# Kernel tuning notes

Measured on AMD Instinct MI355X. Metric: run time of the kernel, lower is better.

## Reference

```python
import jax, jax.numpy as jnp
import numpy as np

# 3x3 laplacian stencil, OIHW
LAP = jnp.array([-1, -1, -1, -1, 8, -1, -1, -1, -1], dtype=jnp.float32).reshape(1, 1, 3, 3)
THR = 0.1
SMOOTH = 1.0


def _lap_conv(x, stride):
    # x: [B,1,H,W]
    return jax.lax.conv_general_dilated(
        x, LAP, window_strides=(stride, stride), padding=((1, 1), (1, 1)),
        dimension_numbers=('NCHW', 'OIHW', 'NCHW'))


def _nearest_up(x, H, W):
    # PyTorch 'nearest': src_idx = floor(dst_idx * in/out)
    h, w = x.shape[2], x.shape[3]
    ri = (jnp.arange(H) * h) // H
    ci = (jnp.arange(W) * w) // W
    return x[:, :, ri][:, :, :, ci]


def _thresh(x):
    return jnp.where(x > THR, 1.0, 0.0).astype(x.dtype)


def setup_inputs() -> dict:
    key = jax.random.key(0)
    k1, k2 = jax.random.split(key)
    B, H, W = 16, 1024, 1024
    boundary_logits = jax.random.normal(k1, (B, 1, H, W), dtype=jnp.float32)
    gtmasks = (jax.random.uniform(k2, (B, H, W)) > 0.5).astype(jnp.float32)
    fuse_kernel = jnp.array([0.6, 0.3, 0.1], dtype=jnp.float32).reshape(1, 3, 1, 1)
    return {"boundary_logits": boundary_logits, "gtmasks": gtmasks, "fuse_kernel": fuse_kernel}


def reference(boundary_logits, gtmasks, fuse_kernel):
    g = gtmasks[:, None, :, :].astype(jnp.float32)  # [B,1,H,W]
    bt = _thresh(jnp.maximum(_lap_conv(g, 1), 0.0))  # full res
    H, W = bt.shape[2], bt.shape[3]
    bt2 = _thresh(_nearest_up(jnp.maximum(_lap_conv(g, 2), 0.0), H, W))
    bt4 = _thresh(_nearest_up(jnp.maximum(_lap_conv(g, 4), 0.0), H, W))
    # (x8 branch in original is computed but unused in the output)
    pyr = jnp.concatenate([bt, bt2, bt4], axis=1)  # [B,3,H,W]
    fused = jnp.einsum('bchw,c->bhw', pyr, fuse_kernel.reshape(3))[:, None]  # 1x1 fuse conv
    target = _thresh(fused)  # [B,1,H,W]

    x = boundary_logits
    # stable BCE with logits, mean reduction
    bce_loss = jnp.mean(jnp.maximum(x, 0.0) - x * target + jnp.log1p(jnp.exp(-jnp.abs(x))))

    p = jax.nn.sigmoid(x)
    n = p.shape[0]
    pf = p.reshape(n, -1)
    tf = target.reshape(n, -1)
    inter = jnp.sum(pf * tf, axis=1)
    dice_loss = jnp.mean(1.0 - (2.0 * inter + SMOOTH) / (jnp.sum(pf, 1) + jnp.sum(tf, 1) + SMOOTH))
    return bce_loss, dice_loss
```

## Files before the change

### kernel.cpp

```cpp
#include <hip/hip_runtime.h>

#define IMG_H 1024
#define IMG_W 1024
#define NIMG  16
#define NPIX  16777216.0f
#define NBLK  2048
#define LOG2E 1.44269504088896340736f
#define LN2   0.69314718055994530942f

#ifndef __has_builtin
#define __has_builtin(x) 0
#endif

__device__ __forceinline__ void stage16(const float* src, float* dstLds, int lane) {
#if __has_builtin(__builtin_amdgcn_global_load_lds)
    __builtin_amdgcn_global_load_lds(
        (const __attribute__((address_space(1))) void*)src,
        (__attribute__((address_space(3))) void*)dstLds,
        16, 0, 0);
#else
    *reinterpret_cast<float4*>(dstLds + (lane << 2)) =
        *reinterpret_cast<const float4*>(src);
#endif
}


__global__ __launch_bounds__(256, 4) void dal_main(
    const float* __restrict__ xlogits,
    const float* __restrict__ gmask,
    const float* __restrict__ fuse,
    float4* __restrict__ ws4)
{
    __shared__ float lds[10 * 1024];

    const int b    = blockIdx.x;
    const int img  = b >> 7;
    const int r0   = (b & 127) << 3;
    const int tid  = (int)threadIdx.x;
    const int wid  = tid >> 6;
    const int lane = tid & 63;
    const int j0   = tid * 4;

    const float w0 = fuse[0], w1 = fuse[1], w2 = fuse[2];

    const size_t ibase = (size_t)img * (IMG_H * IMG_W);
    const float* gi = gmask + ibase;
    const float* xi = xlogits + ibase;

    #pragma unroll
    for (int t = 0; t < 10; ++t) {
        int r  = r0 - 1 + t;
        int rc = r < 0 ? 0 : (r > IMG_H - 1 ? IMG_H - 1 : r);
        stage16(gi + (size_t)rc * IMG_W + j0, &lds[t * 1024 + (wid << 8)], lane);
    }

    float4 xv[8];
    const float* xr = xi + (size_t)r0 * IMG_W + j0;
    #pragma unroll
    for (int r = 0; r < 8; ++r)
        xv[r] = *reinterpret_cast<const float4*>(xr + (size_t)r * IMG_W);

    __syncthreads();

    const bool hasL = (j0 > 0);
    const bool hasR = (j0 + 4 < IMG_W);
    const int  jl   = hasL ? j0 - 1 : 0;
    const int  jr   = hasR ? j0 + 4 : IMG_W - 1;

    auto fold = [&](int t, float* rm, float* cvo) {
        const float* Lr = &lds[t * 1024];
        float4 v   = *reinterpret_cast<const float4*>(Lr + j0);
        float  lf0 = Lr[jl];
        float  rg0 = Lr[jr];
        float  lf  = hasL ? lf0 : 0.f;
        float  rg  = hasR ? rg0 : 0.f;
        rm[0] = fminf(lf,  fminf(v.x, v.y));
        rm[1] = fminf(v.x, fminf(v.y, v.z));
        rm[2] = fminf(v.y, fminf(v.z, v.w));
        rm[3] = fminf(v.z, fminf(v.w, rg));
        cvo[0] = v.x; cvo[1] = v.y; cvo[2] = v.z; cvo[3] = v.w;
    };

    float l2[2]  = {0.f, 0.f}, xt[2] = {0.f, 0.f};
    float itr[2] = {0.f, 0.f}, sp[2] = {0.f, 0.f};
    int st = 0;

    auto px = [&](float x, float btv, float b2v, int a) {
        float f = fmaf(w0, btv, b2v);
        bool  c = f > 0.1f;
        st += (int)__popcll(__ballot(c));
        float u   = __builtin_amdgcn_exp2f(x * LOG2E);
        float opu = 1.f + u;
        float p   = u * __builtin_amdgcn_rcpf(opu);
        l2[a]  += __builtin_amdgcn_logf(opu);
        sp[a]  += p;
        xt[a]  += c ? x : 0.f;
        itr[a] += c ? p : 0.f;
    };

    float rm0[4], rm1[4], rm2[4], rm3[4], cvA[4], cvB[4], cvC[4], tmp[4];
    fold(0, rm0, tmp);
    if (r0 == 0) { rm0[0] = rm0[1] = rm0[2] = rm0[3] = 0.f; }
    fold(1, rm1, cvA);
    float wb4A = 0.f, wb4B = 0.f;

    #pragma unroll
    for (int rp = 0; rp < 4; ++rp) {
        fold(2 * rp + 2, rm2, cvB);
        fold(2 * rp + 3, rm3, cvC);
        if (rp == 3 && r0 == IMG_H - 8) {
            rm3[0] = rm3[1] = rm3[2] = rm3[3] = 0.f;
        }

        float bta[4], btb[4];
        #pragma unroll
        for (int k = 0; k < 4; ++k) {
            float cma = fminf(rm0[k], fminf(rm1[k], rm2[k]));
            float cmb = fminf(rm1[k], fminf(rm2[k], rm3[k]));
            bta[k] = (cvA[k] > 0.5f && cma < 0.5f) ? 1.f : 0.f;
            btb[k] = (cvB[k] > 0.5f && cmb < 0.5f) ? 1.f : 0.f;
        }
        if (rp == 0) wb4A = w2 * bta[0];
        if (rp == 2) wb4B = w2 * bta[0];
        const float wb  = (rp < 2) ? wb4A : wb4B;
        const float b20 = fmaf(w1, bta[0], wb);
        const float b21 = fmaf(w1, bta[2], wb);

        px(xv[2 * rp].x,     bta[0], b20, 0);
        px(xv[2 * rp].y,     bta[1], b20, 0);
        px(xv[2 * rp].z,     bta[2], b21, 0);
        px(xv[2 * rp].w,     bta[3], b21, 0);
        px(xv[2 * rp + 1].x, btb[0], b20, 1);
        px(xv[2 * rp + 1].y, btb[1], b20, 1);
        px(xv[2 * rp + 1].z, btb[2], b21, 1);
        px(xv[2 * rp + 1].w, btb[3], b21, 1);

        #pragma unroll
        for (int k = 0; k < 4; ++k) {
            rm0[k] = rm2[k]; rm1[k] = rm3[k]; cvA[k] = cvC[k];
        }
    }

    float bce   = fmaf(LN2, l2[0] + l2[1], -(xt[0] + xt[1]));
    float inter = itr[0] + itr[1];
    float sump  = sp[0] + sp[1];

    #pragma unroll
    for (int off = 32; off > 0; off >>= 1) {
        bce   += __shfl_down(bce, off);
        inter += __shfl_down(inter, off);
        sump  += __shfl_down(sump, off);
    }
    __syncthreads();
    if (lane == 0) {
        lds[wid]      = bce;
        lds[4 + wid]  = inter;
        lds[8 + wid]  = sump;
        lds[12 + wid] = (float)st;
    }
    __syncthreads();
    if (tid == 0) {
        float4 o;
        o.x = (lds[0]  + lds[1])  + (lds[2]  + lds[3]);
        o.y = (lds[4]  + lds[5])  + (lds[6]  + lds[7]);
        o.z = (lds[8]  + lds[9])  + (lds[10] + lds[11]);
        o.w = (lds[12] + lds[13]) + (lds[14] + lds[15]);
        ws4[b] = o;
    }
}

__global__ __launch_bounds__(1024) void dal_finalize(
    const float4* __restrict__ ws4, float* __restrict__ out)
{
    const int t    = (int)threadIdx.x;
    const int wv   = t >> 6;
    const int lane = t & 63;

    float4 a = ws4[2 * t];
    float4 bq = ws4[2 * t + 1];
    float bce   = a.x + bq.x;
    float inter = a.y + bq.y;
    float sump  = a.z + bq.z;
    float sumt  = a.w + bq.w;

    #pragma unroll
    for (int off = 32; off > 0; off >>= 1) {
        bce   += __shfl_down(bce, off);
        inter += __shfl_down(inter, off);
        sump  += __shfl_down(sump, off);
        sumt  += __shfl_down(sumt, off);
    }

    __shared__ float sb[16], sd[16];
    if (lane == 0) {
        sb[wv] = bce;
        sd[wv] = 1.f - (2.f * inter + 1.f) / (sump + sumt + 1.f);
    }
    __syncthreads();
    if (t == 0) {
        float tb = 0.f, td = 0.f;
        #pragma unroll
        for (int i = 0; i < NIMG; ++i) { tb += sb[i]; td += sd[i]; }
        out[0] = tb / NPIX;
        out[1] = td / (float)NIMG;
    }
}

extern "C" void kernel_launch(void* const* d_in, const int* in_sizes, int n_in,
                              void* d_out, int out_size, void* d_ws, size_t ws_size,
                              hipStream_t stream)
{
    const float* x    = (const float*)d_in[0];
    const float* g    = (const float*)d_in[1];
    const float* fuse = (const float*)d_in[2];
    float* out = (float*)d_out;
    float4* ws4 = (float4*)d_ws;

    dal_main<<<NBLK, 256, 0, stream>>>(x, g, fuse, ws4);
    dal_finalize<<<1, 1024, 0, stream>>>(ws4, out);
}
```

Baseline: 32.09 us.

## Halve rows per block, swizzle blocks across XCDs, raise occupancy

```diff
diff --git a/kernel.cpp b/kernel.cpp
--- a/kernel.cpp
+++ b/kernel.cpp
@@ -4,7 +4,7 @@
 #define IMG_W 1024
 #define NIMG  16
 #define NPIX  16777216.0f
-#define NBLK  2048
+#define NBLK  4096
 #define LOG2E 1.44269504088896340736f
 #define LN2   0.69314718055994530942f
 
@@ -25,17 +25,19 @@
 }
 
 
-__global__ __launch_bounds__(256, 4) void dal_main(
+__global__ __launch_bounds__(256, 6) void dal_main(
     const float* __restrict__ xlogits,
     const float* __restrict__ gmask,
     const float* __restrict__ fuse,
     float4* __restrict__ ws4)
 {
-    __shared__ float lds[10 * 1024];
-
-    const int b    = blockIdx.x;
-    const int img  = b >> 7;
-    const int r0   = (b & 127) << 3;
+    __shared__ float lds[6 * 1024];
+
+    const int bid = blockIdx.x;
+    const int b   = (bid & 7) * (NBLK / 8) + (bid >> 3);
+
+    const int img  = b >> 8;
+    const int r0   = (b & 255) << 2;
     const int tid  = (int)threadIdx.x;
     const int wid  = tid >> 6;
     const int lane = tid & 63;
@@ -48,16 +50,16 @@
     const float* xi = xlogits + ibase;
 
     #pragma unroll
-    for (int t = 0; t < 10; ++t) {
+    for (int t = 0; t < 6; ++t) {
         int r  = r0 - 1 + t;
         int rc = r < 0 ? 0 : (r > IMG_H - 1 ? IMG_H - 1 : r);
         stage16(gi + (size_t)rc * IMG_W + j0, &lds[t * 1024 + (wid << 8)], lane);
     }
 
-    float4 xv[8];
+    float4 xv[4];
     const float* xr = xi + (size_t)r0 * IMG_W + j0;
     #pragma unroll
-    for (int r = 0; r < 8; ++r)
+    for (int r = 0; r < 4; ++r)
         xv[r] = *reinterpret_cast<const float4*>(xr + (size_t)r * IMG_W);
 
     __syncthreads();
@@ -81,6 +83,32 @@
         cvo[0] = v.x; cvo[1] = v.y; cvo[2] = v.z; cvo[3] = v.w;
     };
 
+    float rm[6][4], cv[4][4], tmp[4];
+    fold(0, rm[0], tmp);
+    fold(1, rm[1], cv[0]);
+    fold(2, rm[2], cv[1]);
+    fold(3, rm[3], cv[2]);
+    fold(4, rm[4], cv[3]);
+    fold(5, rm[5], tmp);
+    if (r0 == 0)         { rm[0][0] = rm[0][1] = rm[0][2] = rm[0][3] = 0.f; }
+    if (r0 == IMG_H - 4) { rm[5][0] = rm[5][1] = rm[5][2] = rm[5][3] = 0.f; }
+
+    float bt[4][4];
+    #pragma unroll
+    for (int r = 0; r < 4; ++r)
+        #pragma unroll
+        for (int k = 0; k < 4; ++k) {
+            float cm = fminf(rm[r][k], fminf(rm[r + 1][k], rm[r + 2][k]));
+            bt[r][k] = (cv[r][k] > 0.5f && cm < 0.5f) ? 1.f : 0.f;
+        }
+
+    const float wb4 = w2 * bt[0][0];
+    float base2[2][2];
+    base2[0][0] = fmaf(w1, bt[0][0], wb4);
+    base2[0][1] = fmaf(w1, bt[0][2], wb4);
+    base2[1][0] = fmaf(w1, bt[2][0], wb4);
+    base2[1][1] = fmaf(w1, bt[2][2], wb4);
+
     float l2[2]  = {0.f, 0.f}, xt[2] = {0.f, 0.f};
     float itr[2] = {0.f, 0.f}, sp[2] = {0.f, 0.f};
     int st = 0;
@@ -98,47 +126,14 @@
         itr[a] += c ? p : 0.f;
     };
 
-    float rm0[4], rm1[4], rm2[4], rm3[4], cvA[4], cvB[4], cvC[4], tmp[4];
-    fold(0, rm0, tmp);
-    if (r0 == 0) { rm0[0] = rm0[1] = rm0[2] = rm0[3] = 0.f; }
-    fold(1, rm1, cvA);
-    float wb4A = 0.f, wb4B = 0.f;
-
-    #pragma unroll
-    for (int rp = 0; rp < 4; ++rp) {
-        fold(2 * rp + 2, rm2, cvB);
-        fold(2 * rp + 3, rm3, cvC);
-        if (rp == 3 && r0 == IMG_H - 8) {
-            rm3[0] = rm3[1] = rm3[2] = rm3[3] = 0.f;
-        }
-
-        float bta[4], btb[4];
-        #pragma unroll
-        for (int k = 0; k < 4; ++k) {
-            float cma = fminf(rm0[k], fminf(rm1[k], rm2[k]));
-            float cmb = fminf(rm1[k], fminf(rm2[k], rm3[k]));
-            bta[k] = (cvA[k] > 0.5f && cma < 0.5f) ? 1.f : 0.f;
-            btb[k] = (cvB[k] > 0.5f && cmb < 0.5f) ? 1.f : 0.f;
-        }
-        if (rp == 0) wb4A = w2 * bta[0];
-        if (rp == 2) wb4B = w2 * bta[0];
-        const float wb  = (rp < 2) ? wb4A : wb4B;
-        const float b20 = fmaf(w1, bta[0], wb);
-        const float b21 = fmaf(w1, bta[2], wb);
-
-        px(xv[2 * rp].x,     bta[0], b20, 0);
-        px(xv[2 * rp].y,     bta[1], b20, 0);
-        px(xv[2 * rp].z,     bta[2], b21, 0);
-        px(xv[2 * rp].w,     bta[3], b21, 0);
-        px(xv[2 * rp + 1].x, btb[0], b20, 1);
-        px(xv[2 * rp + 1].y, btb[1], b20, 1);
-        px(xv[2 * rp + 1].z, btb[2], b21, 1);
-        px(xv[2 * rp + 1].w, btb[3], b21, 1);
-
-        #pragma unroll
-        for (int k = 0; k < 4; ++k) {
-            rm0[k] = rm2[k]; rm1[k] = rm3[k]; cvA[k] = cvC[k];
-        }
+    #pragma unroll
+    for (int r = 0; r < 4; ++r) {
+        const float bA = base2[r >> 1][0];
+        const float bB = base2[r >> 1][1];
+        px(xv[r].x, bt[r][0], bA, r & 1);
+        px(xv[r].y, bt[r][1], bA, r & 1);
+        px(xv[r].z, bt[r][2], bB, r & 1);
+        px(xv[r].w, bt[r][3], bB, r & 1);
     }
 
     float bce   = fmaf(LN2, l2[0] + l2[1], -(xt[0] + xt[1]));
@@ -175,13 +170,16 @@
     const int t    = (int)threadIdx.x;
     const int wv   = t >> 6;
     const int lane = t & 63;
-
-    float4 a = ws4[2 * t];
-    float4 bq = ws4[2 * t + 1];
-    float bce   = a.x + bq.x;
-    float inter = a.y + bq.y;
-    float sump  = a.z + bq.z;
-    float sumt  = a.w + bq.w;
+    const int i0   = t * 4;
+
+    float4 a = ws4[i0];
+    float4 b = ws4[i0 + 1];
+    float4 c = ws4[i0 + 2];
+    float4 d = ws4[i0 + 3];
+    float bce   = (a.x + b.x) + (c.x + d.x);
+    float inter = (a.y + b.y) + (c.y + d.y);
+    float sump  = (a.z + b.z) + (c.z + d.z);
+    float sumt  = (a.w + b.w) + (c.w + d.w);
 
     #pragma unroll
     for (int off = 32; off > 0; off >>= 1) {
```

Result: faster. 29.60 us (-7.8%).
